# Kernel optimization log

Hardware: AMD Instinct MI355X
Metric: run time of the kernel (lower is better)

The kernel has to match this reference:

```python
import jax, jax.numpy as jnp
import numpy as np

# ---- geometry / filter constants (from source script) ----
N0, N1, N2 = 16, 200, 200
NUM_RAD, NUM_PHI = 223, 190
VOX = 2.0                      # mm, isotropic voxel size
STEP = 2.0                     # mm, ray sampling step
SCAN_R = 350.0                 # scanner radius -> rays span [-350, 350] mm
NUM_T = int(2 * SCAN_R / STEP) + 1   # 351 samples per ray
SIGMA = 4.5 / (2.35 * VOX)     # gaussian sigma in voxels
RADIUS = int(4.0 * SIGMA + 0.5)      # scipy truncate=4 convention
ORG1 = (-N1 / 2 + 0.5) * VOX
ORG2 = (-N2 / 2 + 0.5) * VOX

_phis = np.linspace(0.0, np.pi, NUM_PHI, endpoint=False, dtype=np.float32)
COS = jnp.asarray(np.cos(_phis), dtype=jnp.float32)
SIN = jnp.asarray(np.sin(_phis), dtype=jnp.float32)
RV = jnp.asarray(np.linspace(-200.0, 200.0, NUM_RAD, dtype=np.float32))
TV = jnp.asarray(np.linspace(-SCAN_R, SCAN_R, NUM_T, dtype=np.float32))
_g = np.exp(-0.5 * (np.arange(-RADIUS, RADIUS + 1) / SIGMA) ** 2)
GW = jnp.asarray((_g / _g.sum()).astype(np.float32))


def _smooth_axis(x, axis):
    pad = [(0, 0)] * x.ndim
    pad[axis] = (RADIUS, RADIUS)
    xp = jnp.pad(x, pad, mode='symmetric')
    n = x.shape[axis]
    return sum(GW[k] * jax.lax.slice_in_dim(xp, k, k + n, axis=axis)
               for k in range(2 * RADIUS + 1))


def gauss3(x):
    # separable 3D gaussian (GaussianFilterOperator)
    for ax in range(3):
        x = _smooth_axis(x, ax)
    return x


def _bilinear(img, ix, iy):
    # img [n0, n1, n2]; ix/iy [num_rad, num_t] fractional voxel coords
    i0 = jnp.floor(ix); j0 = jnp.floor(iy)
    fi = ix - i0; fj = iy - j0
    i0 = i0.astype(jnp.int32); j0 = j0.astype(jnp.int32)
    valid = ((ix >= 0) & (ix <= N1 - 1) & (iy >= 0) & (iy <= N2 - 1)).astype(img.dtype)
    i0c = jnp.clip(i0, 0, N1 - 1); i1c = jnp.clip(i0 + 1, 0, N1 - 1)
    j0c = jnp.clip(j0, 0, N2 - 1); j1c = jnp.clip(j0 + 1, 0, N2 - 1)
    v = ((1 - fi) * (1 - fj) * img[:, i0c, j0c]
         + fi * (1 - fj) * img[:, i1c, j0c]
         + (1 - fi) * fj * img[:, i0c, j1c]
         + fi * fj * img[:, i1c, j1c])          # [n0, num_rad, num_t]
    return v * valid


def project(img):
    # ParallelViewProjector2D: line integrals per slice -> [n0, num_phi, num_rad]
    def body(_, cs):
        c, s = cs
        # ray point = r * perp(phi) + t * dir(phi); perp=(-s,c), dir=(c,s)
        ix = (RV[:, None] * (-s) + TV[None, :] * c - ORG1) / VOX
        iy = (RV[:, None] * c + TV[None, :] * s - ORG2) / VOX
        return None, _bilinear(img, ix, iy).sum(-1) * STEP
    _, sino = jax.lax.scan(body, None, (COS, SIN))   # [num_phi, n0, num_rad]
    return jnp.transpose(sino, (1, 0, 2))


def fwd_model(x, mult):
    # CompositeLinearOperator((sens_mult, projector, gaussian_filter))
    return mult * project(gauss3(x))


def adjoint_model(y, mult, like):
    # exact adjoint of the linear fwd_model via vjp
    _, vjpf = jax.vjp(lambda u: fwd_model(u, mult), jnp.zeros_like(like))
    return vjpf(y)[0]


def setup_inputs() -> dict:
    key = jax.random.key(0)
    k1, k2, k3, k4 = jax.random.split(key, 4)
    x = jax.random.uniform(k1, (N0, N1, N2), dtype=jnp.float32) + 0.1
    data = jax.random.uniform(k2, (N0, NUM_PHI, NUM_RAD), dtype=jnp.float32) * 10.0
    contamination = jax.random.uniform(k3, (N0, NUM_PHI, NUM_RAD), dtype=jnp.float32) * 0.5 + 0.5
    mult = jax.random.uniform(k4, (N0, NUM_PHI, NUM_RAD), dtype=jnp.float32) * 0.5 + 0.5
    ones_sino = jnp.ones((N0, NUM_PHI, NUM_RAD), dtype=jnp.float32)
    sens_image = jnp.maximum(adjoint_model(ones_sino, mult, x), 1e-2)
    return {"x": x, "data": data, "contamination": contamination,
            "mult": mult, "sens_image": sens_image}


def reference(x, data, contamination, mult, sens_image):
    # PoissonEMModule.forward: one MLEM update
    exp = fwd_model(x, mult) + contamination
    return x * adjoint_model(data / exp, mult, x) / sens_image
```

## Files before the change

### kernel.cpp

```cpp
#include <hip/hip_runtime.h>
#include <math.h>

#define N0 16
#define N1 200
#define N2 200
#define NPIX (N1 * N2)
#define NVOX (N0 * NPIX)
#define NUM_RAD 223
#define NUM_PHI 190
#define NUM_T 351
#define NSINO (N0 * NUM_PHI * NUM_RAD)
#define PITCH16 3328
#define S16 (3328 * 210)
#define BASEOFF16 (4 * 3328 + 4 * 16)
#define BP_CHUNK 38
#define BP_NCH 5

__global__ void init_consts(float* __restrict__ cosb, float* __restrict__ sinb,
                            float* __restrict__ rvb, float* __restrict__ gwb) {
    int t = threadIdx.x;
    const double PI = 3.14159265358979311599796346854418516159;
    if (t < NUM_PHI) {
        double step = PI / 190.0;
        float phif = (float)((double)t * step);
        cosb[t] = (float)cos((double)phif);
        sinb[t] = (float)sin((double)phif);
    }
    if (t < NUM_RAD) {
        double step = 400.0 / 222.0;
        float rv = (float)(-200.0 + (double)t * step);
        if (t == NUM_RAD - 1) rv = 200.0f;
        rvb[t] = rv;
    }
    if (t == 0) {
        double sig = 4.5 / (2.35 * 2.0);
        double g[9], ssum = 0.0;
        for (int k = 0; k < 9; ++k) { double d = (double)(k - 4) / sig; g[k] = exp(-0.5 * d * d); ssum += g[k]; }
        for (int k = 0; k < 9; ++k) gwb[k] = (float)(g[k] / ssum);
    }
}

__global__ void smooth_fwd(const float* __restrict__ in, float* __restrict__ out,
                           const float* __restrict__ gwb, int n, int stride) {
    int e = blockIdx.x * 256 + threadIdx.x;
    if (e >= NVOX) return;
    int a = (e / stride) % n;
    int base = e - a * stride;
    float sum = 0.f;
#pragma unroll
    for (int k = 0; k < 9; ++k) {
        int q = a + k - 4;
        q = (q < 0) ? (-1 - q) : ((q >= n) ? (2 * n - 1 - q) : q);
        sum = __fadd_rn(sum, __fmul_rn(gwb[k], in[base + q * stride]));
    }
    out[e] = sum;
}

__global__ void smooth_fwd2_16(const float* __restrict__ in, float* __restrict__ P16,
                               float* __restrict__ PT16, const float* __restrict__ gwb) {
    int t = blockIdx.x * 256 + threadIdx.x;
    if (t >= 2 * NPIX) return;
    int oct = t & 1;
    int pix = t >> 1;
    int i1 = pix / N2;
    int i2 = pix - i1 * N2;
    int rowbase = i1 * N2;
    float v[8];
#pragma unroll
    for (int jj = 0; jj < 8; ++jj) {
        int i0 = oct * 8 + jj;
        const float* tin = in + i0 * NPIX + rowbase;
        float sum = 0.f;
#pragma unroll
        for (int k = 0; k < 9; ++k) {
            int q = i2 + k - 4;
            q = (q < 0) ? (-1 - q) : ((q >= N2) ? (2 * N2 - 1 - q) : q);
            sum = __fadd_rn(sum, __fmul_rn(gwb[k], tin[q]));
        }
        v[jj] = sum;
    }
    int po  = BASEOFF16 + i1 * PITCH16 + i2 * 16 + oct * 8;
    int pto = BASEOFF16 + i2 * PITCH16 + i1 * 16 + oct * 8;
    *(float4*)(P16 + po)      = make_float4(v[0], v[1], v[2], v[3]);
    *(float4*)(P16 + po + 4)  = make_float4(v[4], v[5], v[6], v[7]);
    *(float4*)(PT16 + pto)     = make_float4(v[0], v[1], v[2], v[3]);
    *(float4*)(PT16 + pto + 4) = make_float4(v[4], v[5], v[6], v[7]);
}

__device__ __forceinline__ float adj_u(const float* __restrict__ in, const float* __restrict__ gwb,
                                       int base, int stride, int n, int j) {
    float r = 0.f;
#pragma unroll
    for (int k = 0; k < 9; ++k) {
        int i = j - k;
        if (i >= 0 && i < n) r = __fadd_rn(r, __fmul_rn(gwb[k], in[base + i * stride]));
    }
    return r;
}

__global__ void smooth_adj(const float* __restrict__ in, float* __restrict__ out,
                           const float* __restrict__ gwb, int n, int stride) {
    int e = blockIdx.x * 256 + threadIdx.x;
    if (e >= NVOX) return;
    int a = (e / stride) % n;
    int base = e - a * stride;
    float v = adj_u(in, gwb, base, stride, n, a + 4);
    if (a < 4)      v = __fadd_rn(v, adj_u(in, gwb, base, stride, n, 3 - a));
    if (a >= n - 4) v = __fadd_rn(v, adj_u(in, gwb, base, stride, n, 2 * n + 3 - a));
    out[e] = v;
}

__device__ __forceinline__ float sum5_at(const float* __restrict__ a, const float* __restrict__ b,
                                         const float* __restrict__ c, const float* __restrict__ d,
                                         const float* __restrict__ e5, int i) {
    return __fadd_rn(__fadd_rn(__fadd_rn(a[i], b[i]), __fadd_rn(c[i], d[i])), e5[i]);
}

__device__ __forceinline__ float adj_u5(const float* __restrict__ a, const float* __restrict__ b,
                                        const float* __restrict__ c, const float* __restrict__ d,
                                        const float* __restrict__ e5, const float* __restrict__ gwb,
                                        int base, int n, int j) {
    float r = 0.f;
#pragma unroll
    for (int k = 0; k < 9; ++k) {
        int i = j - k;
        if (i >= 0 && i < n) r = __fadd_rn(r, __fmul_rn(gwb[k], sum5_at(a, b, c, d, e5, base + i)));
    }
    return r;
}

__global__ void smooth_adj2_sum5(const float* __restrict__ a, const float* __restrict__ b,
                                 const float* __restrict__ c, const float* __restrict__ d,
                                 const float* __restrict__ e5, const float* __restrict__ gwb,
                                 float* __restrict__ out) {
    int e = blockIdx.x * 256 + threadIdx.x;
    if (e >= NVOX) return;
    int i2 = e % N2;
    int base = e - i2;
    float v = adj_u5(a, b, c, d, e5, gwb, base, N2, i2 + 4);
    if (i2 < 4)       v = __fadd_rn(v, adj_u5(a, b, c, d, e5, gwb, base, N2, 3 - i2));
    if (i2 >= N2 - 4) v = __fadd_rn(v, adj_u5(a, b, c, d, e5, gwb, base, N2, 2 * N2 + 3 - i2));
    out[e] = v;
}

__global__ void smooth_adj0_final(const float* __restrict__ in, const float* __restrict__ x,
                                  const float* __restrict__ sens, const float* __restrict__ gwb,
                                  float* __restrict__ out) {
    int e = blockIdx.x * 256 + threadIdx.x;
    if (e >= NVOX) return;
    int a = e / NPIX;
    int base = e - a * NPIX;
    float v = adj_u(in, gwb, base, NPIX, N0, a + 4);
    if (a < 4)  v = __fadd_rn(v, adj_u(in, gwb, base, NPIX, N0, 3 - a));
    if (a >= 12) v = __fadd_rn(v, adj_u(in, gwb, base, NPIX, N0, 35 - a));
    out[e] = __fdiv_rn(__fmul_rn(x[e], v), sens[e]);
}

template<bool USET>
__device__ __forceinline__ void geom2(float tv, float ch, float sh, float Ah, float Bh,
                                      float& w00, float& w10, float& w01, float& w11,
                                      int& o) {
    float ix = fmaf(tv, ch, Ah);
    float iy = fmaf(tv, sh, Bh);
    bool valid = (ix >= 0.f) & (ix <= 199.f) & (iy >= 0.f) & (iy <= 199.f);
    float fx = floorf(ix), fy = floorf(iy);
    int ii = (int)fx, jj = (int)fy;
    float fi = ix - fx, fj = iy - fy;
    int rowi = USET ? jj : ii;
    int coli = USET ? ii : jj;
    o = rowi * PITCH16 + coli * 16;
    float gi = 1.f - fi, gj = 1.f - fj;
    w00 = valid ? gi * gj : 0.f;
    w10 = valid ? fi * gj : 0.f;
    w01 = valid ? gi * fj : 0.f;
    w11 = valid ? fi * fj : 0.f;
}

template<bool USET>
__device__ __forceinline__ void ray_loop(const float* __restrict__ basep,
                                         int kbeg, int kend, float ch, float sh,
                                         float Ah, float Bh, float sums[4]) {
    constexpr int O10 = USET ? 16 : PITCH16;
    constexpr int O01 = USET ? PITCH16 : 16;
    float tv = (float)(2 * kbeg - 350);
    float w00, w10, w01, w11;
    int o;
    geom2<USET>(tv, ch, sh, Ah, Bh, w00, w10, w01, w11, o);
    float4 L00 = *(const float4*)(basep + o);
    float4 L10 = *(const float4*)(basep + o + O10);
    float4 L01 = *(const float4*)(basep + o + O01);
    float4 L11 = *(const float4*)(basep + o + O10 + O01);
#pragma unroll 2
    for (int k = kbeg; k < kend; ++k) {
        tv += 2.0f;
        float nw00, nw10, nw01, nw11;
        int no;
        geom2<USET>(tv, ch, sh, Ah, Bh, nw00, nw10, nw01, nw11, no);
        float4 N00 = *(const float4*)(basep + no);
        float4 N10 = *(const float4*)(basep + no + O10);
        float4 N01 = *(const float4*)(basep + no + O01);
        float4 N11 = *(const float4*)(basep + no + O10 + O01);
        sums[0] = fmaf(w00, L00.x, sums[0]); sums[0] = fmaf(w10, L10.x, sums[0]);
        sums[0] = fmaf(w01, L01.x, sums[0]); sums[0] = fmaf(w11, L11.x, sums[0]);
        sums[1] = fmaf(w00, L00.y, sums[1]); sums[1] = fmaf(w10, L10.y, sums[1]);
        sums[1] = fmaf(w01, L01.y, sums[1]); sums[1] = fmaf(w11, L11.y, sums[1]);
        sums[2] = fmaf(w00, L00.z, sums[2]); sums[2] = fmaf(w10, L10.z, sums[2]);
        sums[2] = fmaf(w01, L01.z, sums[2]); sums[2] = fmaf(w11, L11.z, sums[2]);
        sums[3] = fmaf(w00, L00.w, sums[3]); sums[3] = fmaf(w10, L10.w, sums[3]);
        sums[3] = fmaf(w11, L11.w, sums[3]); sums[3] = fmaf(w01, L01.w, sums[3]);
        w00 = nw00; w10 = nw10; w01 = nw01; w11 = nw11;
        L00 = N00; L10 = N10; L01 = N01; L11 = N11;
        __builtin_amdgcn_sched_group_barrier(0x002, 24, 0);
        __builtin_amdgcn_sched_group_barrier(0x020, 4, 0);
        __builtin_amdgcn_sched_group_barrier(0x002, 16, 0);
    }
    sums[0] = fmaf(w00, L00.x, sums[0]); sums[0] = fmaf(w10, L10.x, sums[0]);
    sums[0] = fmaf(w01, L01.x, sums[0]); sums[0] = fmaf(w11, L11.x, sums[0]);
    sums[1] = fmaf(w00, L00.y, sums[1]); sums[1] = fmaf(w10, L10.y, sums[1]);
    sums[1] = fmaf(w01, L01.y, sums[1]); sums[1] = fmaf(w11, L11.y, sums[1]);
    sums[2] = fmaf(w00, L00.z, sums[2]); sums[2] = fmaf(w10, L10.z, sums[2]);
    sums[2] = fmaf(w01, L01.z, sums[2]); sums[2] = fmaf(w11, L11.z, sums[2]);
    sums[3] = fmaf(w00, L00.w, sums[3]); sums[3] = fmaf(w10, L10.w, sums[3]);
    sums[3] = fmaf(w01, L01.w, sums[3]); sums[3] = fmaf(w11, L11.w, sums[3]);
}

__global__ __launch_bounds__(512, 2)
void project_ratio(const float* __restrict__ P16, const float* __restrict__ PT16,
                   const float* __restrict__ data,
                   const float* __restrict__ contam, const float* __restrict__ mult,
                   const float* __restrict__ cosb, const float* __restrict__ sinb,
                   const float* __restrict__ rvb, float* __restrict__ zt) {
    int b = blockIdx.x;
    int sw = (b & 7) * 95 + (b >> 3);
    int rc  = sw & 3;
    int phi = sw >> 2;
    int tx = threadIdx.x;
    int chunk = tx & 3;
    int rr = tx >> 2;
    int r = rc * 64 + rr;
    int half = threadIdx.y;
    bool active = (r < NUM_RAD);

    __shared__ float part[4][256];

    float sums[4] = {0.f, 0.f, 0.f, 0.f};
    float c = cosb[phi], sp = sinb[phi];
    float ch = c * 0.5f, sh = sp * 0.5f;

    bool useT = fabsf(sp) > fabsf(c);
    const float* basep = (useT ? PT16 : P16) + BASEOFF16 + chunk * 4;

    if (active) {
        float rv = rvb[r];
        float A = __fmul_rn(rv, -sp);
        float B = __fmul_rn(rv, c);
        float Ah = fmaf(rv, -sh, 99.5f);
        float Bh = fmaf(rv, ch, 99.5f);

        float tlo = -350.f, thi = 350.f;
        bool empty = false;
        if (fabsf(c) > 1e-6f) {
            float a0 = (-199.f - A) / c, b0 = (199.f - A) / c;
            tlo = fmaxf(tlo, fminf(a0, b0)); thi = fminf(thi, fmaxf(a0, b0));
        } else if (fabsf(A) > 199.5f) empty = true;
        if (fabsf(sp) > 1e-6f) {
            float a0 = (-199.f - B) / sp, b0 = (199.f - B) / sp;
            tlo = fmaxf(tlo, fminf(a0, b0)); thi = fminf(thi, fmaxf(a0, b0));
        } else if (fabsf(B) > 199.5f) empty = true;

        int klo = max(0, (int)floorf((tlo + 350.f) * 0.5f) - 1);
        int khi = min(NUM_T - 1, (int)ceilf((thi + 350.f) * 0.5f) + 1);

        if (!empty && klo <= khi) {
            int kmid = (klo + khi + 1) >> 1;
            int kbeg = half ? kmid : klo;
            int kend = half ? khi : (kmid - 1);
            if (kbeg <= kend) {
                if (useT) ray_loop<true>(basep, kbeg, kend, ch, sh, Ah, Bh, sums);
                else      ray_loop<false>(basep, kbeg, kend, ch, sh, Ah, Bh, sums);
            }
        }
    }

    if (half == 1) {
#pragma unroll
        for (int s = 0; s < 4; ++s) part[s][tx] = sums[s];
    }
    __syncthreads();
    if (half == 0 && active) {
#pragma unroll
        for (int s = 0; s < 4; ++s) {
            float proj = __fmul_rn(__fadd_rn(sums[s], part[s][tx]), 2.0f);
            int sl = chunk * 4 + s;
            int idx = (sl * NUM_PHI + phi) * NUM_RAD + r;
            float ex = __fadd_rn(__fmul_rn(mult[idx], proj), contam[idx]);
            float zval = __fmul_rn(mult[idx], __fdiv_rn(data[idx], ex));
            zt[(phi * NUM_RAD + r) * N0 + sl] = zval;
        }
    }
}

__global__ __launch_bounds__(256, 6)
void backproject(const float* __restrict__ zt, const float* __restrict__ cosb,
                 const float* __restrict__ sinb, const float* __restrict__ rvb,
                 float* __restrict__ q0, float* __restrict__ q1, float* __restrict__ q2,
                 float* __restrict__ q3, float* __restrict__ q4) {
    int tx = threadIdx.x;
    int q = tx & 3;
    int pix = blockIdx.x * 64 + (tx >> 2);
    int pc = blockIdx.y;
    int i1 = pix / N2;
    int i2 = pix - i1 * N2;
    float X1 = 2.f * (float)i1 - 199.f;
    float X2 = 2.f * (float)i2 - 199.f;
    float i1f = (float)i1, i2f = (float)i2;
    int lb = tx & 60;
    float acc[4] = {0.f, 0.f, 0.f, 0.f};

    int p_end = pc * BP_CHUNK + BP_CHUNK;
    for (int p = pc * BP_CHUNK; p < p_end; ++p) {
        float c = cosb[p], sp = sinb[p];
        float ch = c * 0.5f, sh = sp * 0.5f;
        float tp = c * X1 + sp * X2;
        float rp = c * X2 - sp * X1;
        int j0 = (int)floorf((rp + 200.f) * 0.555f);
        int jb = min(max(j0 - 1, 0), NUM_RAD - 4);
        float tc = (tp + 350.f) * 0.5f;
        int kc = (int)floorf(tc + 0.5f);

        const float4* zb = (const float4*)(zt + (p * NUM_RAD + jb) * N0);
        float4 Z0 = zb[q];
        float4 Z1 = zb[4 + q];
        float4 Z2 = zb[8 + q];
        float4 Z3 = zb[12 + q];

        float tvc = (float)(2 * kc - 350);
        float Qx[3], Qy[3];
#pragma unroll
        for (int dk = 0; dk < 3; ++dk) {
            float tv = tvc + (float)(2 * (dk - 1));
            Qx[dk] = fmaf(tv, ch, 99.5f);
            Qy[dk] = fmaf(tv, sh, 99.5f);
        }
        float rvj = rvb[jb + q];
        float Px = rvj * (-sh);
        float Py = rvj * ch;
        float w = 0.f;
#pragma unroll
        for (int dk = 0; dk < 3; ++dk) {
            float ix = Px + Qx[dk];
            float iy = Py + Qy[dk];
            bool valid = (ix >= 0.f) & (ix <= 199.f) & (iy >= 0.f) & (iy <= 199.f);
            float wx = fmaxf(0.f, 1.f - fabsf(ix - i1f));
            float wy = fmaxf(0.f, 1.f - fabsf(iy - i2f));
            float wxm = valid ? wx : 0.f;
            w = fmaf(wxm, wy, w);
        }

        float w0 = __shfl(w, lb + 0);
        float w1 = __shfl(w, lb + 1);
        float w2 = __shfl(w, lb + 2);
        float w3 = __shfl(w, lb + 3);

        acc[0] = fmaf(w0, Z0.x, acc[0]); acc[1] = fmaf(w0, Z0.y, acc[1]);
        acc[2] = fmaf(w0, Z0.z, acc[2]); acc[3] = fmaf(w0, Z0.w, acc[3]);
        acc[0] = fmaf(w1, Z1.x, acc[0]); acc[1] = fmaf(w1, Z1.y, acc[1]);
        acc[2] = fmaf(w1, Z1.z, acc[2]); acc[3] = fmaf(w1, Z1.w, acc[3]);
        acc[0] = fmaf(w2, Z2.x, acc[0]); acc[1] = fmaf(w2, Z2.y, acc[1]);
        acc[2] = fmaf(w2, Z2.z, acc[2]); acc[3] = fmaf(w2, Z2.w, acc[3]);
        acc[0] = fmaf(w3, Z3.x, acc[0]); acc[1] = fmaf(w3, Z3.y, acc[1]);
        acc[2] = fmaf(w3, Z3.z, acc[2]); acc[3] = fmaf(w3, Z3.w, acc[3]);
    }

    float* pp = (pc == 0) ? q0 : (pc == 1) ? q1 : (pc == 2) ? q2 : (pc == 3) ? q3 : q4;
#pragma unroll
    for (int i = 0; i < 4; ++i)
        pp[(q * 4 + i) * NPIX + pix] = acc[i] * 2.0f;
}

extern "C" void kernel_launch(void* const* d_in, const int* in_sizes, int n_in,
                              void* d_out, int out_size, void* d_ws, size_t ws_size,
                              hipStream_t stream) {
    const float* x      = (const float*)d_in[0];
    const float* data   = (const float*)d_in[1];
    const float* contam = (const float*)d_in[2];
    const float* mult   = (const float*)d_in[3];
    const float* sens   = (const float*)d_in[4];
    float* out = (float*)d_out;

    float* W    = (float*)d_ws;
    float* s    = W;
    float* tmp  = W + NVOX;
    float* bp2  = W + 2 * NVOX;
    float* zt   = W + 3 * NVOX;
    float* P16  = W + 3 * NVOX + NSINO;
    float* PT16 = P16 + S16;
    float* cosb = PT16 + S16;
    float* sinb = cosb + NUM_PHI;
    float* rvb  = sinb + NUM_PHI;
    float* gwb  = rvb + NUM_RAD;

    hipLaunchKernelGGL(init_consts, dim3(1), dim3(256), 0, stream, cosb, sinb, rvb, gwb);

    int nb = (NVOX + 255) / 256;
    hipLaunchKernelGGL(smooth_fwd, dim3(nb), dim3(256), 0, stream, x,   s,   gwb, N0, NPIX);
    hipLaunchKernelGGL(smooth_fwd, dim3(nb), dim3(256), 0, stream, s,   tmp, gwb, N1, N2);
    int nb2 = (2 * NPIX + 255) / 256;
    hipLaunchKernelGGL(smooth_fwd2_16, dim3(nb2), dim3(256), 0, stream, tmp, P16, PT16, gwb);

    hipLaunchKernelGGL(project_ratio, dim3(NUM_PHI * 4), dim3(256, 2), 0, stream,
                       P16, PT16, data, contam, mult, cosb, sinb, rvb, zt);

    hipLaunchKernelGGL(backproject, dim3(NPIX / 64, BP_NCH), dim3(256), 0, stream,
                       zt, cosb, sinb, rvb, s, tmp, bp2, P16, PT16);

    hipLaunchKernelGGL(smooth_adj2_sum5, dim3(nb), dim3(256), 0, stream,
                       s, tmp, bp2, P16, PT16, gwb, zt);
    hipLaunchKernelGGL(smooth_adj, dim3(nb), dim3(256), 0, stream, zt, s, gwb, N1, N2);
    hipLaunchKernelGGL(smooth_adj0_final, dim3(nb), dim3(256), 0, stream, s, x, sens, gwb, out);
}
```

Measured before the change: 273.3 us.

## Split projection rays into four t-segments per block and shrink radial tile

The projection kernel now gives each block 32 radial bins across 4 thread rows, each covering a quarter of the ray's sample range, instead of 64 bins split into two halves. The four partial sums are reduced through shared memory, and the grid becomes 2D (7 x 190) without the old block swizzle. Launch bounds ask for 8 blocks per CU to raise occupancy and latency hiding. The cost is more shared-memory reduction work, 7x32=224 radial slots with little waste, and possible register pressure or spills at the higher occupancy target.

```diff
diff --git a/kernel.cpp b/kernel.cpp
--- a/kernel.cpp
+++ b/kernel.cpp
@@ -207,7 +207,7 @@
         sums[2] = fmaf(w00, L00.z, sums[2]); sums[2] = fmaf(w10, L10.z, sums[2]);
         sums[2] = fmaf(w01, L01.z, sums[2]); sums[2] = fmaf(w11, L11.z, sums[2]);
         sums[3] = fmaf(w00, L00.w, sums[3]); sums[3] = fmaf(w10, L10.w, sums[3]);
-        sums[3] = fmaf(w11, L11.w, sums[3]); sums[3] = fmaf(w01, L01.w, sums[3]);
+        sums[3] = fmaf(w01, L01.w, sums[3]); sums[3] = fmaf(w11, L11.w, sums[3]);
         w00 = nw00; w10 = nw10; w01 = nw01; w11 = nw11;
         L00 = N00; L10 = N10; L01 = N01; L11 = N11;
         __builtin_amdgcn_sched_group_barrier(0x002, 24, 0);
@@ -224,24 +224,22 @@
     sums[3] = fmaf(w01, L01.w, sums[3]); sums[3] = fmaf(w11, L11.w, sums[3]);
 }
 
-__global__ __launch_bounds__(512, 2)
+__global__ __launch_bounds__(512, 8)
 void project_ratio(const float* __restrict__ P16, const float* __restrict__ PT16,
                    const float* __restrict__ data,
                    const float* __restrict__ contam, const float* __restrict__ mult,
                    const float* __restrict__ cosb, const float* __restrict__ sinb,
                    const float* __restrict__ rvb, float* __restrict__ zt) {
-    int b = blockIdx.x;
-    int sw = (b & 7) * 95 + (b >> 3);
-    int rc  = sw & 3;
-    int phi = sw >> 2;
+    int rc  = blockIdx.x;
+    int phi = blockIdx.y;
     int tx = threadIdx.x;
+    int ty = threadIdx.y;
     int chunk = tx & 3;
     int rr = tx >> 2;
-    int r = rc * 64 + rr;
-    int half = threadIdx.y;
+    int r = rc * 32 + rr;
     bool active = (r < NUM_RAD);
 
-    __shared__ float part[4][256];
+    __shared__ float part[4][4][128];
 
     float sums[4] = {0.f, 0.f, 0.f, 0.f};
     float c = cosb[phi], sp = sinb[phi];
@@ -272,9 +270,9 @@
         int khi = min(NUM_T - 1, (int)ceilf((thi + 350.f) * 0.5f) + 1);
 
         if (!empty && klo <= khi) {
-            int kmid = (klo + khi + 1) >> 1;
-            int kbeg = half ? kmid : klo;
-            int kend = half ? khi : (kmid - 1);
+            int klen = khi - klo + 1;
+            int kbeg = klo + ((ty * klen) >> 2);
+            int kend = klo + (((ty + 1) * klen) >> 2) - 1;
             if (kbeg <= kend) {
                 if (useT) ray_loop<true>(basep, kbeg, kend, ch, sh, Ah, Bh, sums);
                 else      ray_loop<false>(basep, kbeg, kend, ch, sh, Ah, Bh, sums);
@@ -282,15 +280,15 @@
         }
     }
 
-    if (half == 1) {
-#pragma unroll
-        for (int s = 0; s < 4; ++s) part[s][tx] = sums[s];
-    }
+#pragma unroll
+    for (int s = 0; s < 4; ++s) part[ty][s][tx] = sums[s];
     __syncthreads();
-    if (half == 0 && active) {
+    if (ty == 0 && active) {
 #pragma unroll
         for (int s = 0; s < 4; ++s) {
-            float proj = __fmul_rn(__fadd_rn(sums[s], part[s][tx]), 2.0f);
+            float v = __fadd_rn(__fadd_rn(__fadd_rn(part[0][s][tx], part[1][s][tx]),
+                                          part[2][s][tx]), part[3][s][tx]);
+            float proj = __fmul_rn(v, 2.0f);
             int sl = chunk * 4 + s;
             int idx = (sl * NUM_PHI + phi) * NUM_RAD + r;
             float ex = __fadd_rn(__fmul_rn(mult[idx], proj), contam[idx]);
@@ -408,7 +406,7 @@
     int nb2 = (2 * NPIX + 255) / 256;
     hipLaunchKernelGGL(smooth_fwd2_16, dim3(nb2), dim3(256), 0, stream, tmp, P16, PT16, gwb);
 
-    hipLaunchKernelGGL(project_ratio, dim3(NUM_PHI * 4), dim3(256, 2), 0, stream,
+    hipLaunchKernelGGL(project_ratio, dim3(7, NUM_PHI), dim3(128, 4), 0, stream,
                        P16, PT16, data, contam, mult, cosb, sinb, rvb, zt);
 
     hipLaunchKernelGGL(backproject, dim3(NPIX / 64, BP_NCH), dim3(256), 0, stream,
```

New measurement: 311.8 us. +14.1%, slower.
